# Performance work log

Measured on AMD Instinct MI355X. Metric: run time of the kernel, lower is better.

## Reference

```python
import jax, jax.numpy as jnp
import numpy as np

B, FEAT, FIELD, K = 16384, 2048, 32, 64

def setup_inputs() -> dict:
    key = jax.random.key(0)
    k1, k2, k3, k4 = jax.random.split(key, 4)
    x = jax.random.normal(k1, (B, FEAT), dtype=jnp.float32)
    # nn.Linear(feature_size, 1): weight [1, FEAT] (use vector), bias [1] (scalar)
    w = jax.random.normal(k2, (FEAT,), dtype=jnp.float32) / np.sqrt(FEAT)
    b = jax.random.normal(k3, (), dtype=jnp.float32)
    # v ~ N(0, 0.01) as in torch.normal(0, 0.01, ...)
    v = 0.01 * jax.random.normal(k4, (FEAT, FIELD, K), dtype=jnp.float32)
    return {"x": x, "w": w, "b": b, "v": v}

def reference(x, w, b, v):
    # linear part: Linear(feature_size, 1).squeeze() -> [B]
    linear_part = x @ w + b  # [B]
    # field_x = tensordot(x, v, dims=1) -> [B, FIELD, K]
    field_x = jnp.einsum('bf,fsk->bsk', x, v)
    # sum_{i<j} sum_k f_i * f_j  ==  0.5 * (||sum_i f_i||^2 - sum_i ||f_i||^2)
    s = field_x.sum(axis=1)                      # [B, K]
    sq = (field_x * field_x).sum(axis=(1, 2))    # [B]
    interaction = 0.5 * ((s * s).sum(axis=-1) - sq)  # [B]
    return jax.nn.sigmoid(linear_part + interaction)
```

## Files before the change

### kernel.cpp

```cpp
#include <hip/hip_runtime.h>
#include <cstdint>
#include <cstddef>

#define B_ROWS 16384
#define FEAT   2048
#define FIELD  32
#define KDIM   64
#define NCOLS  2048
#define NAUG   2176

using half8   = __attribute__((ext_vector_type(8))) _Float16;
using half4   = __attribute__((ext_vector_type(4))) _Float16;
using floatx4 = __attribute__((ext_vector_type(4))) float;

__device__ __forceinline__ void load_lds16(const void* g, void* l) {
  __builtin_amdgcn_global_load_lds((const __attribute__((address_space(1))) void*)g,
                                   (__attribute__((address_space(3))) void*)l, 16, 0, 0);
}

__global__ __launch_bounds__(256) void k_prep_x(const float* __restrict__ x,
                                                _Float16* __restrict__ xh) {
  const int bb = blockIdx.x;
  const int t = threadIdx.x;
  size_t i = ((size_t)bb * 256 + t) * 16;
  float4 v0 = *(const float4*)(x + i);
  float4 v1 = *(const float4*)(x + i + 4);
  float4 v2 = *(const float4*)(x + i + 8);
  float4 v3 = *(const float4*)(x + i + 12);
  half8 h0 = { (_Float16)v0.x, (_Float16)v0.y, (_Float16)v0.z, (_Float16)v0.w,
               (_Float16)v1.x, (_Float16)v1.y, (_Float16)v1.z, (_Float16)v1.w };
  half8 h1 = { (_Float16)v2.x, (_Float16)v2.y, (_Float16)v2.z, (_Float16)v2.w,
               (_Float16)v3.x, (_Float16)v3.y, (_Float16)v3.z, (_Float16)v3.w };
  *(half8*)(xh + i) = h0;
  *(half8*)(xh + i + 8) = h1;
}

__global__ __launch_bounds__(256) void k_prep_v(const float* __restrict__ v,
                                                const float* __restrict__ w,
                                                _Float16* __restrict__ vt,
                                                float* __restrict__ arg) {
  const int bb = blockIdx.x;
  const int t = threadIdx.x;
  if (bb < 1024) {
    __shared__ _Float16 tile[64 * 68];
    const int f0 = (bb >> 5) * 64;
    const int n0 = (bb & 31) * 64;
#pragma unroll
    for (int j = 0; j < 4; ++j) {
      int c = j * 256 + t;
      int row = c >> 4;
      int col = (c & 15) * 4;
      float4 val = *(const float4*)(v + (size_t)(f0 + row) * NCOLS + n0 + col);
      tile[row * 68 + col + 0] = (_Float16)val.x;
      tile[row * 68 + col + 1] = (_Float16)val.y;
      tile[row * 68 + col + 2] = (_Float16)val.z;
      tile[row * 68 + col + 3] = (_Float16)val.w;
    }
    __syncthreads();
#pragma unroll
    for (int j = 0; j < 4; ++j) {
      int c = j * 256 + t;
      int nl = c >> 4;
      int fl = (c & 15) * 4;
      half4 h = { tile[(fl + 0) * 68 + nl], tile[(fl + 1) * 68 + nl],
                  tile[(fl + 2) * 68 + nl], tile[(fl + 3) * 68 + nl] };
      *(half4*)(vt + (size_t)(n0 + nl) * FEAT + f0 + fl) = h;
    }
  } else if (bb < 1536) {
    const int k = t & 63;
    const int f = (bb - 1024) * 4 + (t >> 6);
    float s = 0.f;
#pragma unroll
    for (int si = 0; si < FIELD; ++si) s += v[(size_t)f * NCOLS + si * KDIM + k];
    vt[(size_t)(NCOLS + k) * FEAT + f] = (_Float16)s;
  } else if (bb < 2048) {
    int idx = (bb - 1536) * 256 + t;
    int r = NCOLS + KDIM + (idx >> 11);
    int f = idx & 2047;
    vt[(size_t)r * FEAT + f] = (r == NCOLS + KDIM) ? (_Float16)w[f] : (_Float16)0.f;
  } else {
    arg[(bb - 2048) * 256 + t] = 0.f;
  }
}

__global__ __launch_bounds__(512, 2) void k_gemm(const _Float16* __restrict__ xh,
                                                 const _Float16* __restrict__ vt,
                                                 float* __restrict__ arg) {
  __shared__ __align__(16) _Float16 lds[65536];
  const int tid  = threadIdx.x;
  const int lane = tid & 63;
  const int wave = tid >> 6;
  const int wm   = wave >> 2;
  const int wn   = wave & 3;
  const int lr   = lane & 15;
  const int q    = lane >> 4;

  const int bid = blockIdx.x;
  const int wg  = (bid & 7) * 72 + (bid >> 3);
  const int ng  = wg / 192;
  const int rem = wg - ng * 192;
  const int mi  = rem / 3;
  const int nr  = rem - mi * 3;
  const int m0  = mi * 256;
  const int n0  = (ng * 3 + nr) * 256;

  int offA[4], offB[4];
#pragma unroll
  for (int f = 0; f < 4; ++f) {
    int L = f * 16 + lr;
    int u = wm * 4 + q;
    offA[f] = L * 64 + ((u ^ (L & 7)) * 8);
  }
#pragma unroll
  for (int g = 0; g < 4; ++g) {
    int L = (wn & 1) * 64 + g * 16 + lr;
    int u = (wn >> 1) * 4 + q;
    offB[g] = L * 64 + ((u ^ (L & 7)) * 8);
  }

  const int L0   = tid >> 3;
  const int u0   = (tid & 7) ^ (L0 & 7);
  const int row0 = (u0 >> 2) * 128 + L0;
  const int kc0  = u0 & 3;
  const _Float16* pA0 = xh + (size_t)(m0 + row0) * FEAT + kc0 * 8;
  const _Float16* pA1 = pA0 + (size_t)64 * FEAT;
  const int rb0 = (n0 + row0      < NAUG) ? n0 + row0      : NAUG - 1;
  const int rb1 = (n0 + row0 + 64 < NAUG) ? n0 + row0 + 64 : NAUG - 1;
  const _Float16* pB0 = vt + (size_t)rb0 * FEAT + kc0 * 8;
  const _Float16* pB1 = vt + (size_t)rb1 * FEAT + kc0 * 8;

  auto stageA = [&](int koff, int seg) {
    load_lds16(pA0 + koff, lds + seg + tid * 8);
    load_lds16(pA1 + koff, lds + seg + 4096 + tid * 8);
  };
  auto stageB = [&](int koff, int seg) {
    load_lds16(pB0 + koff, lds + seg + tid * 8);
    load_lds16(pB1 + koff, lds + seg + 4096 + tid * 8);
  };

  floatx4 acc[8][4] = {};
  half8 af[4], bf[4];

  stageA(0, 0);       stageB(0, 32768);
  stageA(32, 8192);   stageB(32, 40960);
  stageA(64, 16384);  stageB(64, 49152);
  asm volatile("s_waitcnt vmcnt(4)" ::: "memory");
  __builtin_amdgcn_s_barrier();

#define PHASE_TAIL()                                        \
    __builtin_amdgcn_s_barrier();                           \
    asm volatile("s_waitcnt lgkmcnt(0)" ::: "memory");      \
    __builtin_amdgcn_sched_barrier(0);                      \
    __builtin_amdgcn_s_setprio(1)

#define PHASE_END()                                         \
    __builtin_amdgcn_s_setprio(0);                          \
    __builtin_amdgcn_s_barrier()

#pragma unroll 2
  for (int t = 0; t < 32; ++t) {
    const int sA0  = ((t & 1) << 1) * 8192;
    const int sB0  = 32768 + sA0;
    const int sPA1 = ((((t + 1) & 1) << 1) | 1) * 8192;

#pragma unroll
    for (int g = 0; g < 4; ++g) bf[g] = *(const half8*)(lds + sB0 + offB[g]);
#pragma unroll
    for (int f = 0; f < 4; ++f) af[f] = *(const half8*)(lds + sA0 + offA[f]);
    if (t < 31) stageA((t + 1) * 64 + 32, sPA1);
    PHASE_TAIL();
#pragma unroll
    for (int f = 0; f < 4; ++f)
#pragma unroll
      for (int g = 0; g < 4; ++g)
        acc[f][g] = __builtin_amdgcn_mfma_f32_16x16x32_f16(af[f], bf[g],
                                                           acc[f][g], 0, 0, 0);
    PHASE_END();

#pragma unroll
    for (int f = 0; f < 4; ++f) af[f] = *(const half8*)(lds + sA0 + 4096 + offA[f]);
    if (t < 31) stageB((t + 1) * 64 + 32, 32768 + sPA1);
    PHASE_TAIL();
#pragma unroll
    for (int f = 0; f < 4; ++f)
#pragma unroll
      for (int g = 0; g < 4; ++g)
        acc[4 + f][g] = __builtin_amdgcn_mfma_f32_16x16x32_f16(af[f], bf[g],
                                                               acc[4 + f][g], 0, 0, 0);
    PHASE_END();

#pragma unroll
    for (int g = 0; g < 4; ++g) bf[g] = *(const half8*)(lds + sB0 + 8192 + offB[g]);
#pragma unroll
    for (int f = 0; f < 4; ++f) af[f] = *(const half8*)(lds + sA0 + 8192 + offA[f]);
    if (t < 30) stageA((t + 2) * 64, sA0);
    PHASE_TAIL();
#pragma unroll
    for (int f = 0; f < 4; ++f)
#pragma unroll
      for (int g = 0; g < 4; ++g)
        acc[f][g] = __builtin_amdgcn_mfma_f32_16x16x32_f16(af[f], bf[g],
                                                           acc[f][g], 0, 0, 0);
    PHASE_END();

#pragma unroll
    for (int f = 0; f < 4; ++f) af[f] = *(const half8*)(lds + sA0 + 12288 + offA[f]);
    if (t < 30) stageB((t + 2) * 64, sB0);
    __builtin_amdgcn_s_barrier();
    asm volatile("s_waitcnt lgkmcnt(0)" ::: "memory");
    __builtin_amdgcn_sched_barrier(0);
    __builtin_amdgcn_s_setprio(1);
#pragma unroll
    for (int f = 0; f < 4; ++f)
#pragma unroll
      for (int g = 0; g < 4; ++g)
        acc[4 + f][g] = __builtin_amdgcn_mfma_f32_16x16x32_f16(af[f], bf[g],
                                                               acc[4 + f][g], 0, 0, 0);
    __builtin_amdgcn_s_setprio(0);
    if (t < 30) { asm volatile("s_waitcnt vmcnt(4)" ::: "memory"); }
    else        { asm volatile("s_waitcnt vmcnt(0)" ::: "memory"); }
    __builtin_amdgcn_sched_barrier(0);
    __builtin_amdgcn_s_barrier();
  }
#undef PHASE_TAIL
#undef PHASE_END

  const int cq = lane >> 4;
  const int mrow = m0 + wm * 128;
  const int ncol = n0 + wn * 64;
#pragma unroll
  for (int f = 0; f < 8; ++f) {
#pragma unroll
    for (int r = 0; r < 4; ++r) {
      float contrib = 0.f;
#pragma unroll
      for (int g = 0; g < 4; ++g) {
        int col = ncol + g * 16 + lr;
        float vv = acc[f][g][r];
        float qv = vv * vv;
        if (col < NCOLS)                contrib -= 0.5f * qv;
        else if (col < NCOLS + KDIM)    contrib += 0.5f * qv;
        else if (col == NCOLS + KDIM)   contrib += vv;
      }
      contrib += __shfl_xor(contrib, 1);
      contrib += __shfl_xor(contrib, 2);
      contrib += __shfl_xor(contrib, 4);
      contrib += __shfl_xor(contrib, 8);
      if (lr == 0) atomicAdd(&arg[mrow + f * 16 + cq * 4 + r], contrib);
    }
  }
}

__global__ __launch_bounds__(256) void k_fin(const float* __restrict__ arg,
                                             const float* __restrict__ b,
                                             float* __restrict__ out) {
  int i = blockIdx.x * 256 + threadIdx.x;
  float z = arg[i] + b[0];
  out[i] = 1.f / (1.f + __expf(-z));
}

extern "C" void kernel_launch(void* const* d_in, const int* in_sizes, int n_in,
                              void* d_out, int out_size, void* d_ws, size_t ws_size,
                              hipStream_t stream) {
  const float* x = (const float*)d_in[0];
  const float* w = (const float*)d_in[1];
  const float* b = (const float*)d_in[2];
  const float* v = (const float*)d_in[3];
  float* out = (float*)d_out;

  char* ws = (char*)d_ws;
  _Float16* xh  = (_Float16*)ws;
  _Float16* vt  = (_Float16*)(ws + 67108864);
  float*    arg = (float*)(ws + 67108864 + 8912896);

  k_prep_x<<<8192, 256, 0, stream>>>(x, xh);
  k_prep_v<<<2112, 256, 0, stream>>>(v, w, vt, arg);
  k_gemm<<<576, 512, 0, stream>>>(xh, vt, arg);
  k_fin<<<64, 256, 0, stream>>>(arg, b, out);
}
```

Measured before the change: 395.6 us.

## Split augmented columns out of main GEMM into fused finalize kernel

The main GEMM previously covered 2176 augmented columns (2048 field columns plus the K-sum and linear columns) in 9 column tiles, so the last tile was mostly padding. It now covers exactly 2048 columns with 512 blocks, which drops the per-column branch in the epilogue and the row clamping. The extra 128 augmented columns (sum over fields and the linear weight) are computed by a small separate MFMA kernel that also applies the bias and sigmoid. The cost is re-reading all of x in fp16 for that narrow GEMM, with a simple unpipelined loop.

```diff
diff --git a/kernel.cpp b/kernel.cpp
--- a/kernel.cpp
+++ b/kernel.cpp
@@ -96,13 +96,13 @@
   const int q    = lane >> 4;
 
   const int bid = blockIdx.x;
-  const int wg  = (bid & 7) * 72 + (bid >> 3);
-  const int ng  = wg / 192;
-  const int rem = wg - ng * 192;
-  const int mi  = rem / 3;
-  const int nr  = rem - mi * 3;
+  const int wg  = (bid & 7) * 64 + (bid >> 3);
+  const int ng  = wg >> 7;
+  const int rem = wg & 127;
+  const int mi  = rem >> 1;
+  const int nr  = rem & 1;
   const int m0  = mi * 256;
-  const int n0  = (ng * 3 + nr) * 256;
+  const int n0  = (ng * 2 + nr) * 256;
 
   int offA[4], offB[4];
 #pragma unroll
@@ -124,10 +124,8 @@
   const int kc0  = u0 & 3;
   const _Float16* pA0 = xh + (size_t)(m0 + row0) * FEAT + kc0 * 8;
   const _Float16* pA1 = pA0 + (size_t)64 * FEAT;
-  const int rb0 = (n0 + row0      < NAUG) ? n0 + row0      : NAUG - 1;
-  const int rb1 = (n0 + row0 + 64 < NAUG) ? n0 + row0 + 64 : NAUG - 1;
-  const _Float16* pB0 = vt + (size_t)rb0 * FEAT + kc0 * 8;
-  const _Float16* pB1 = vt + (size_t)rb1 * FEAT + kc0 * 8;
+  const _Float16* pB0 = vt + (size_t)(n0 + row0) * FEAT + kc0 * 8;
+  const _Float16* pB1 = pB0 + (size_t)64 * FEAT;
 
   auto stageA = [&](int koff, int seg) {
     load_lds16(pA0 + koff, lds + seg + tid * 8);
@@ -227,7 +225,6 @@
 
   const int cq = lane >> 4;
   const int mrow = m0 + wm * 128;
-  const int ncol = n0 + wn * 64;
 #pragma unroll
   for (int f = 0; f < 8; ++f) {
 #pragma unroll
@@ -235,12 +232,8 @@
       float contrib = 0.f;
 #pragma unroll
       for (int g = 0; g < 4; ++g) {
-        int col = ncol + g * 16 + lr;
         float vv = acc[f][g][r];
-        float qv = vv * vv;
-        if (col < NCOLS)                contrib -= 0.5f * qv;
-        else if (col < NCOLS + KDIM)    contrib += 0.5f * qv;
-        else if (col == NCOLS + KDIM)   contrib += vv;
+        contrib -= 0.5f * vv * vv;
       }
       contrib += __shfl_xor(contrib, 1);
       contrib += __shfl_xor(contrib, 2);
@@ -251,12 +244,92 @@
   }
 }
 
-__global__ __launch_bounds__(256) void k_fin(const float* __restrict__ arg,
-                                             const float* __restrict__ b,
-                                             float* __restrict__ out) {
-  int i = blockIdx.x * 256 + threadIdx.x;
-  float z = arg[i] + b[0];
-  out[i] = 1.f / (1.f + __expf(-z));
+__global__ __launch_bounds__(256) void k_fin_aug(const _Float16* __restrict__ xh,
+                                                 const _Float16* __restrict__ vt,
+                                                 const float* __restrict__ arg,
+                                                 const float* __restrict__ b,
+                                                 float* __restrict__ out) {
+  __shared__ __align__(16) _Float16 lds_a[64 * 64];
+  __shared__ __align__(16) _Float16 lds_b[128 * 64];
+  __shared__ float augp[64];
+  const int t = threadIdx.x;
+  const int m0 = blockIdx.x * 64;
+  const int lane = t & 63;
+  const int wave = t >> 6;
+  const int wm = (wave & 1) * 32;
+  const int wn = (wave >> 1) * 64;
+  const int lr = lane & 15;
+  const int lk = (lane >> 4) * 8;
+
+  if (t < 64) augp[t] = 0.f;
+
+  floatx4 acc[2][4] = {};
+
+  for (int k0 = 0; k0 < FEAT; k0 += 64) {
+#pragma unroll
+    for (int i = 0; i < 2; ++i) {
+      int c = i * 256 + t;
+      int row = c >> 3;
+      int g = (c & 7) ^ (row & 7);
+      load_lds16(xh + (size_t)(m0 + row) * FEAT + k0 + g * 8, lds_a + c * 8);
+    }
+#pragma unroll
+    for (int i = 0; i < 4; ++i) {
+      int c = i * 256 + t;
+      int row = c >> 3;
+      int g = (c & 7) ^ (row & 7);
+      load_lds16(vt + (size_t)(NCOLS + row) * FEAT + k0 + g * 8, lds_b + c * 8);
+    }
+    __syncthreads();
+#pragma unroll
+    for (int ks = 0; ks < 64; ks += 32) {
+      const int kc = (ks + lk) >> 3;
+      half8 af[2], bf[4];
+#pragma unroll
+      for (int f = 0; f < 2; ++f) {
+        int ma = wm + f * 16 + lr;
+        af[f] = *(const half8*)(lds_a + ma * 64 + (kc ^ (ma & 7)) * 8);
+      }
+#pragma unroll
+      for (int f = 0; f < 4; ++f) {
+        int nb = wn + f * 16 + lr;
+        bf[f] = *(const half8*)(lds_b + nb * 64 + (kc ^ (nb & 7)) * 8);
+      }
+#pragma unroll
+      for (int fm = 0; fm < 2; ++fm)
+#pragma unroll
+        for (int fn = 0; fn < 4; ++fn)
+          acc[fm][fn] = __builtin_amdgcn_mfma_f32_16x16x32_f16(af[fm], bf[fn],
+                                                               acc[fm][fn], 0, 0, 0);
+    }
+    __syncthreads();
+  }
+
+  const int cq = lane >> 4;
+#pragma unroll
+  for (int fm = 0; fm < 2; ++fm) {
+#pragma unroll
+    for (int r = 0; r < 4; ++r) {
+      float contrib = 0.f;
+#pragma unroll
+      for (int fn = 0; fn < 4; ++fn) {
+        int col = wn + fn * 16 + lr;
+        float vv = acc[fm][fn][r];
+        if (col < KDIM)            contrib += 0.5f * vv * vv;
+        else if (col == KDIM)      contrib += vv;
+      }
+      contrib += __shfl_xor(contrib, 1);
+      contrib += __shfl_xor(contrib, 2);
+      contrib += __shfl_xor(contrib, 4);
+      contrib += __shfl_xor(contrib, 8);
+      if (lr == 0) atomicAdd(&augp[wm + fm * 16 + cq * 4 + r], contrib);
+    }
+  }
+  __syncthreads();
+  if (t < 64) {
+    float z = arg[m0 + t] + augp[t] + b[0];
+    out[m0 + t] = 1.f / (1.f + __expf(-z));
+  }
 }
 
 extern "C" void kernel_launch(void* const* d_in, const int* in_sizes, int n_in,
@@ -275,6 +348,6 @@
 
   k_prep_x<<<8192, 256, 0, stream>>>(x, xh);
   k_prep_v<<<2112, 256, 0, stream>>>(v, w, vt, arg);
-  k_gemm<<<576, 512, 0, stream>>>(xh, vt, arg);
-  k_fin<<<64, 256, 0, stream>>>(arg, b, out);
-}
+  k_gemm<<<512, 512, 0, stream>>>(xh, vt, arg);
+  k_fin_aug<<<256, 256, 0, stream>>>(xh, vt, arg, b, out);
+}
```

New measurement: 374.7 us. -5.3%, faster.
